# Performance work log

Measured on AMD Instinct MI355X. Metric: run time of the kernel, lower is better.

The kernel has to match this reference:

```python
import jax, jax.numpy as jnp
import numpy as np

B, H, U, C, K = 256, 1024, 1024, 512, 10

def setup_inputs() -> dict:
    key = jax.random.key(0)
    k1, k2, k3, k4, k5 = jax.random.split(key, 5)
    h = jax.random.normal(k1, (B, H), dtype=jnp.float32)
    c_seq = jax.random.normal(k2, (B, U, C), dtype=jnp.float32)
    k_prev = jax.random.uniform(k3, (B, K), dtype=jnp.float32)
    # Linear(hidden, 3K) params, PyTorch default init: U(-1/sqrt(H), 1/sqrt(H))
    bound = 1.0 / np.sqrt(H)
    W = jax.random.uniform(k4, (3 * K, H), dtype=jnp.float32, minval=-bound, maxval=bound)
    b = jax.random.uniform(k5, (3 * K,), dtype=jnp.float32, minval=-bound, maxval=bound)
    return {"h": h, "c_seq": c_seq, "k_prev": k_prev, "W": W, "b": b}

def reference(h, c_seq, k_prev, W, b):
    params = h @ W.T + b                      # [B, 3K]
    alpha, beta, kappa = jnp.split(params, 3, axis=1)
    alpha = jax.nn.softplus(alpha) + 1e-4     # [B, K]
    beta = jnp.clip(jax.nn.softplus(beta), 0.1, 10.0)
    kappa = k_prev + jax.nn.softplus(kappa) * 0.1
    u = jnp.arange(c_seq.shape[1], dtype=jnp.float32)[None, None, :]  # [1,1,U]
    # Gaussian mixture window weights, summed over K components
    phi = jnp.sum(alpha[:, :, None] * jnp.exp(-beta[:, :, None] * (kappa[:, :, None] - u) ** 2), axis=1)  # [B, U]
    window = jnp.einsum('bu,buc->bc', phi, c_seq)  # [B, C]
    return (window, phi, kappa)
```

## Files before the change

### kernel.cpp

```cpp
#include <hip/hip_runtime.h>
#include <math.h>

#define BB 256
#define HH 1024
#define UU 1024
#define CC 512
#define KK 10

#define EXP_CUTOFF 110.0f

__device__ __forceinline__ float softplus_f(float x) {
    return fmaxf(x, 0.0f) + log1pf(expf(-fabsf(x)));
}

__global__ void softwindow_fused(const float* __restrict__ h,
                                 const float* __restrict__ c_seq,
                                 const float* __restrict__ k_prev,
                                 const float* __restrict__ W,
                                 const float* __restrict__ bias,
                                 float* __restrict__ window,
                                 float* __restrict__ phi_out,
                                 float* __restrict__ kappa_out) {
    __shared__ float sh[HH];
    __shared__ float sphi[UU];
    __shared__ float sparams[3 * KK];
    __shared__ float sa[KK], sb[KK], sk[KK];
    __shared__ float sbound[KK];
    __shared__ int s_hi;

    const int b = blockIdx.x;
    const int t = threadIdx.x;

    ((float4*)sh)[t] = ((const float4*)(h + (size_t)b * HH))[t];
    __syncthreads();

    const int wave = t >> 6;
    const int lane = t & 63;
    for (int j = wave; j < 3 * KK; j += 4) {
        const float* wrow = W + (size_t)j * HH;
        float sum = 0.0f;
        #pragma unroll
        for (int l = lane; l < HH; l += 64) sum += sh[l] * wrow[l];
        #pragma unroll
        for (int off = 32; off > 0; off >>= 1) sum += __shfl_down(sum, off);
        if (lane == 0) sparams[j] = sum + bias[j];
    }
    __syncthreads();

    if (t < KK) {
        float a  = softplus_f(sparams[t]) + 1e-4f;
        float be = fminf(fmaxf(softplus_f(sparams[KK + t]), 0.1f), 10.0f);
        float ka = k_prev[b * KK + t] + softplus_f(sparams[2 * KK + t]) * 0.1f;
        sa[t] = a;
        sb[t] = be;
        sk[t] = ka;
        kappa_out[b * KK + t] = ka;
        sbound[t] = ka + sqrtf(EXP_CUTOFF / be);
    }
    __syncthreads();
    if (t == 0) {
        float mb = sbound[0];
        #pragma unroll
        for (int k = 1; k < KK; ++k) mb = fmaxf(mb, sbound[k]);
        int hi = (mb < 0.0f) ? 0 : (int)ceilf(mb) + 1;
        s_hi = hi > UU ? UU : hi;
    }
    __syncthreads();

    #pragma unroll
    for (int i = 0; i < UU / 256; ++i) {
        const int u = t + i * 256;
        const float uf = (float)u;
        float p = 0.0f;
        #pragma unroll
        for (int k = 0; k < KK; ++k) {
            const float d = sk[k] - uf;
            p += sa[k] * __expf(-sb[k] * d * d);
        }
        sphi[u] = p;
        phi_out[(size_t)b * UU + u] = p;
    }
    __syncthreads();

    const int hi = s_hi;
    const float2* base = (const float2*)(c_seq + (size_t)b * UU * CC);
    float2 acc = {0.0f, 0.0f};
    int u = 0;
    for (; u + 4 <= hi; u += 4) {
        #pragma unroll
        for (int j = 0; j < 4; ++j) {
            const float p = sphi[u + j];
            const float2 v = base[(size_t)(u + j) * (CC / 2) + t];
            acc.x += p * v.x;
            acc.y += p * v.y;
        }
    }
    for (; u < hi; ++u) {
        const float p = sphi[u];
        const float2 v = base[(size_t)u * (CC / 2) + t];
        acc.x += p * v.x;
        acc.y += p * v.y;
    }
    ((float2*)(window + (size_t)b * CC))[t] = acc;
}

extern "C" void kernel_launch(void* const* d_in, const int* in_sizes, int n_in,
                              void* d_out, int out_size, void* d_ws, size_t ws_size,
                              hipStream_t stream) {
    const float* h      = (const float*)d_in[0];
    const float* c_seq  = (const float*)d_in[1];
    const float* k_prev = (const float*)d_in[2];
    const float* W      = (const float*)d_in[3];
    const float* bias   = (const float*)d_in[4];

    float* out     = (float*)d_out;
    float* window  = out;
    float* phi     = out + BB * CC;
    float* kappa_o = out + BB * CC + BB * UU;

    softwindow_fused<<<BB, 256, 0, stream>>>(h, c_seq, k_prev, W, bias,
                                             window, phi, kappa_o);
}
```

Measured before the change: 620.9 us.

## Batch GEMV rows per wave and split window reduction over u with float4 loads

The projection GEMV now has each wave compute eight output rows at once from one float4 load of h, which cuts repeated shared-memory reads and adds independent accumulators. The window reduction uses float4 loads of c_seq, with the two half-blocks splitting u by parity and combining partial sums through shared memory. A launch_bounds hint is also added. The aim is more memory-level parallelism on the c_seq stream, at the cost of an extra barrier and higher register pressure.

```diff
diff --git a/kernel.cpp b/kernel.cpp
--- a/kernel.cpp
+++ b/kernel.cpp
@@ -13,20 +13,22 @@
     return fmaxf(x, 0.0f) + log1pf(expf(-fabsf(x)));
 }
 
-__global__ void softwindow_fused(const float* __restrict__ h,
-                                 const float* __restrict__ c_seq,
-                                 const float* __restrict__ k_prev,
-                                 const float* __restrict__ W,
-                                 const float* __restrict__ bias,
-                                 float* __restrict__ window,
-                                 float* __restrict__ phi_out,
-                                 float* __restrict__ kappa_out) {
+__global__ __launch_bounds__(256, 1)
+void softwindow_fused(const float* __restrict__ h,
+                      const float* __restrict__ c_seq,
+                      const float* __restrict__ k_prev,
+                      const float* __restrict__ W,
+                      const float* __restrict__ bias,
+                      float* __restrict__ window,
+                      float* __restrict__ phi_out,
+                      float* __restrict__ kappa_out) {
     __shared__ float sh[HH];
     __shared__ float sphi[UU];
     __shared__ float sparams[3 * KK];
     __shared__ float sa[KK], sb[KK], sk[KK];
     __shared__ float sbound[KK];
     __shared__ int s_hi;
+    __shared__ float4 spart[CC / 4];
 
     const int b = blockIdx.x;
     const int t = threadIdx.x;
@@ -36,14 +38,34 @@
 
     const int wave = t >> 6;
     const int lane = t & 63;
-    for (int j = wave; j < 3 * KK; j += 4) {
-        const float* wrow = W + (size_t)j * HH;
-        float sum = 0.0f;
+    const int j0 = wave * 8;
+
+    float sums[8];
+    #pragma unroll
+    for (int r = 0; r < 8; ++r) sums[r] = 0.0f;
+
+    const float4* sh4 = (const float4*)sh;
+    #pragma unroll
+    for (int i = 0; i < HH / 256; ++i) {
+        const float4 hv = sh4[lane + 64 * i];
         #pragma unroll
-        for (int l = lane; l < HH; l += 64) sum += sh[l] * wrow[l];
+        for (int r = 0; r < 8; ++r) {
+            int jj = j0 + r;
+            if (jj > 3 * KK - 1) jj = 3 * KK - 1;
+            const float4 wv = ((const float4*)(W + (size_t)jj * HH))[lane + 64 * i];
+            sums[r] = fmaf(hv.x, wv.x, sums[r]);
+            sums[r] = fmaf(hv.y, wv.y, sums[r]);
+            sums[r] = fmaf(hv.z, wv.z, sums[r]);
+            sums[r] = fmaf(hv.w, wv.w, sums[r]);
+        }
+    }
+    #pragma unroll
+    for (int r = 0; r < 8; ++r) {
+        float s = sums[r];
         #pragma unroll
-        for (int off = 32; off > 0; off >>= 1) sum += __shfl_down(sum, off);
-        if (lane == 0) sparams[j] = sum + bias[j];
+        for (int off = 32; off > 0; off >>= 1) s += __shfl_down(s, off);
+        const int jj = j0 + r;
+        if (lane == 0 && jj < 3 * KK) sparams[jj] = s + bias[jj];
     }
     __syncthreads();
 
@@ -83,25 +105,26 @@
     __syncthreads();
 
     const int hi = s_hi;
-    const float2* base = (const float2*)(c_seq + (size_t)b * UU * CC);
-    float2 acc = {0.0f, 0.0f};
-    int u = 0;
-    for (; u + 4 <= hi; u += 4) {
-        #pragma unroll
-        for (int j = 0; j < 4; ++j) {
-            const float p = sphi[u + j];
-            const float2 v = base[(size_t)(u + j) * (CC / 2) + t];
-            acc.x += p * v.x;
-            acc.y += p * v.y;
-        }
+    const int col  = t & 127;
+    const int half = t >> 7;
+    const float4* base4 = (const float4*)(c_seq + (size_t)b * UU * CC);
+    float4 acc = {0.0f, 0.0f, 0.0f, 0.0f};
+    #pragma unroll 4
+    for (int u = half; u < hi; u += 2) {
+        const float p = sphi[u];
+        const float4 v = base4[(size_t)u * (CC / 4) + col];
+        acc.x = fmaf(p, v.x, acc.x);
+        acc.y = fmaf(p, v.y, acc.y);
+        acc.z = fmaf(p, v.z, acc.z);
+        acc.w = fmaf(p, v.w, acc.w);
     }
-    for (; u < hi; ++u) {
-        const float p = sphi[u];
-        const float2 v = base[(size_t)u * (CC / 2) + t];
-        acc.x += p * v.x;
-        acc.y += p * v.y;
+    if (half) spart[col] = acc;
+    __syncthreads();
+    if (!half) {
+        const float4 o = spart[col];
+        acc.x += o.x; acc.y += o.y; acc.z += o.z; acc.w += o.w;
+        ((float4*)(window + (size_t)b * CC))[col] = acc;
     }
-    ((float2*)(window + (size_t)b * CC))[t] = acc;
 }
 
 extern "C" void kernel_launch(void* const* d_in, const int* in_sizes, int n_in,
```

New measurement: 576.5 us. 7.2% less time.
